# Performance work log

Measured on AMD Instinct MI355X. Metric: run time of the kernel, lower is better.

## Reference

```python
import jax, jax.numpy as jnp
import numpy as np

N_NODES = 20000
NEG_SLOPE = 0.2  # PyG GATConv default leaky_relu slope


def segment_softmax(e, dst, num_segments):
    # e: [E, H] edge logits, softmax over edges sharing the same dst node
    m = jax.ops.segment_max(e, dst, num_segments=num_segments)
    ex = jnp.exp(e - m[dst])
    s = jax.ops.segment_sum(ex, dst, num_segments=num_segments)
    return ex / (s[dst] + 1e-16)


def gat_conv(x, src, dst, W, att_src, att_dst, bias, concat):
    # PyG GATConv (add_self_loops handled by caller). W: [Fin, H*C], att_*: [H, C]
    N = x.shape[0]
    H, C = att_src.shape
    h = (x @ W).reshape(N, H, C)
    a_src = jnp.einsum('nhc,hc->nh', h, att_src)  # [N, H]
    a_dst = jnp.einsum('nhc,hc->nh', h, att_dst)
    e = jax.nn.leaky_relu(a_src[src] + a_dst[dst], NEG_SLOPE)  # [E, H]
    alpha = segment_softmax(e, dst, N)
    msg = alpha[:, :, None] * h[src]  # [E, H, C]
    out = jax.ops.segment_sum(msg, dst, num_segments=N)  # [N, H, C]
    out = out.reshape(N, H * C) if concat else out.mean(axis=1)
    return out + bias


def add_self_loops(edge_index, num_nodes):
    loops = jnp.arange(num_nodes, dtype=edge_index.dtype)
    src = jnp.concatenate([edge_index[0], loops])
    dst = jnp.concatenate([edge_index[1], loops])
    return src, dst


def setup_inputs() -> dict:
    key = jax.random.key(0)
    ks = jax.random.split(key, 24)
    Fin, Hd, Hh, C2, Md = 1280, 256, 4, 128, 1024

    def w(k, shape, fan_in):
        return (jax.random.normal(k, shape, jnp.float32) * (1.0 / np.sqrt(fan_in))).astype(jnp.float32)

    return {
        'x': jax.random.normal(ks[0], (N_NODES, Fin), jnp.float32),
        'edge_index': jax.random.randint(ks[1], (2, 200000), 0, N_NODES, jnp.int32),
        'mutation_idx': 12345,
        'mutation_site_diff': jax.random.normal(ks[2], (1, Md), jnp.float32),
        # mutation_diff_processor: 1024 -> 128 -> 128
        'W_mut1': w(ks[3], (Md, 128), Md), 'b_mut1': jnp.zeros((128,), jnp.float32),
        'W_mut2': w(ks[4], (128, 128), 128), 'b_mut2': jnp.zeros((128,), jnp.float32),
        # GATConv1: Fin -> 256, 4 heads, concat
        'gat1_W': w(ks[5], (Fin, Hh * Hd), Fin),
        'gat1_as': w(ks[6], (Hh, Hd), Hd), 'gat1_ad': w(ks[7], (Hh, Hd), Hd),
        'gat1_b': jnp.zeros((Hh * Hd,), jnp.float32),
        # GATConv2: 1024 -> 128, 1 head
        'gat2_W': w(ks[8], (Hh * Hd, C2), Hh * Hd),
        'gat2_as': w(ks[9], (1, C2), C2), 'gat2_ad': w(ks[10], (1, C2), C2),
        'gat2_b': jnp.zeros((C2,), jnp.float32),
        # binding_predictor: 256 -> 128 -> 32 -> 1
        'W_p1': w(ks[11], (C2 + 128, 128), C2 + 128), 'b_p1': jnp.zeros((128,), jnp.float32),
        'W_p2': w(ks[12], (128, 32), 128), 'b_p2': jnp.zeros((32,), jnp.float32),
        'W_p3': w(ks[13], (32, 1), 32), 'b_p3': jnp.zeros((1,), jnp.float32),
    }


def reference(x, edge_index, mutation_idx, mutation_site_diff,
              W_mut1, b_mut1, W_mut2, b_mut2,
              gat1_W, gat1_as, gat1_ad, gat1_b,
              gat2_W, gat2_as, gat2_ad, gat2_b,
              W_p1, b_p1, W_p2, b_p2, W_p3, b_p3):
    src, dst = add_self_loops(edge_index, x.shape[0])
    # mutation diff MLP (dropout = identity at eval)
    pmd = jax.nn.relu(mutation_site_diff @ W_mut1 + b_mut1) @ W_mut2 + b_mut2
    h = jax.nn.relu(gat_conv(x, src, dst, gat1_W, gat1_as, gat1_ad, gat1_b, concat=True))
    h = jax.nn.relu(gat_conv(h, src, dst, gat2_W, gat2_as, gat2_ad, gat2_b, concat=False))
    feat = h[mutation_idx:mutation_idx + 1]  # [1, 128]
    z = jnp.concatenate([feat, pmd], axis=-1)
    z = jax.nn.relu(z @ W_p1 + b_p1)
    z = jax.nn.relu(z @ W_p2 + b_p2)
    return z @ W_p3 + b_p3
```

## Files before the change

### kernel.cpp

```cpp
#include <hip/hip_runtime.h>
#include <hip/hip_bf16.h>

#define NNODES 20000
#define NE_RAW 200000
#define NE_TOT 220000
#define MAX1   128
#define MAXE1  4096
#define MAXE2  256
#define FIN    1280
#define FH     1024
#define NHEAD  4
#define C2     128
#define CAPE   512
#define KCK    64
#define NKC    20
#define INIT_B 79
#define A_B    160
#define PMD_B  4
#define D_B    160

__device__ __forceinline__ float lrelu(float x){ return x >= 0.f ? x : 0.2f * x; }

__global__ __launch_bounds__(256) void k_init_a(
    const float* __restrict__ W1, const float* __restrict__ as1,
    const float* __restrict__ ad1,
    const float* __restrict__ msd, const float* __restrict__ Wm1,
    const float* __restrict__ bm1,
    int* cnt, int* slot1, float* __restrict__ w_att, float* __restrict__ r1){
  int t = threadIdx.x, b = blockIdx.x;
  if (b < INIT_B){
    int i = b * 256 + t;
    if (i < NNODES) slot1[i] = -1;
    if (i < 8) cnt[i] = 0;
    return;
  }
  if (b >= INIT_B + A_B){
    __shared__ float red[256];
    int pb  = b - INIT_B - A_B;
    int col = pb * 32 + (t & 31);
    int sl  = t >> 5;
    float s = 0.f;
    for (int k = sl * 128; k < sl * 128 + 128; ++k)
      s += msd[k] * Wm1[k * C2 + col];
    red[t] = s;
    __syncthreads();
    if (t < 32){
      float v = 0.f;
      #pragma unroll
      for (int q = 0; q < 8; ++q) v += red[q * 32 + t];
      v += bm1[col];
      r1[col] = v > 0.f ? v : 0.f;
    }
    return;
  }
  __shared__ float red[4][8];
  int kbase = (b - INIT_B) * 8;
  int w = t >> 6, lane = t & 63;
  float av0 = as1[t], av1 = as1[t + 256], av2 = as1[t + 512], av3 = as1[t + 768];
  float dv0 = ad1[t], dv1 = ad1[t + 256], dv2 = ad1[t + 512], dv3 = ad1[t + 768];
  for (int rr = 0; rr < 8; ++rr){
    int k = kbase + rr;
    const float* Wr = W1 + (long)k * FH;
    float w0 = Wr[t], w1 = Wr[t + 256], w2 = Wr[t + 512], w3 = Wr[t + 768];
    float v[8] = { w0*av0, w1*av1, w2*av2, w3*av3, w0*dv0, w1*dv1, w2*dv2, w3*dv3 };
    #pragma unroll
    for (int q = 0; q < 8; ++q){
      float s = v[q];
      #pragma unroll
      for (int o = 32; o; o >>= 1) s += __shfl_xor(s, o, 64);
      if (lane == 0) red[w][q] = s;
      __syncthreads();
      if (t == 0) w_att[k * 8 + q] = red[0][q] + red[1][q] + red[2][q] + red[3][q];
      __syncthreads();
    }
  }
}

__global__ void k_scan1(const int* __restrict__ ei, const int* __restrict__ mip,
                        int* cnt, int* slot1, int* S1, int* E2){
  int e0 = (blockIdx.x * 256 + threadIdx.x) * 4;
  if (e0 >= NE_TOT) return;
  int mi = mip[0];
  int s[4], d[4], n = 0;
  if (e0 + 3 < NE_RAW){
    int4 s4 = *(const int4*)(ei + e0);
    int4 d4 = *(const int4*)(ei + NE_RAW + e0);
    s[0]=s4.x; s[1]=s4.y; s[2]=s4.z; s[3]=s4.w;
    d[0]=d4.x; d[1]=d4.y; d[2]=d4.z; d[3]=d4.w;
    n = 4;
  } else {
    for (int q = 0; q < 4; ++q){
      int e = e0 + q;
      if (e >= NE_TOT) break;
      if (e < NE_RAW){ s[n] = ei[e]; d[n] = ei[NE_RAW + e]; }
      else { s[n] = e - NE_RAW; d[n] = s[n]; }
      ++n;
    }
  }
  for (int q = 0; q < n; ++q){
    if (d[q] != mi) continue;
    int p = atomicAdd(&cnt[3], 1);
    if (p < MAXE2) E2[p] = s[q];
    if (atomicCAS(&slot1[s[q]], -1, -9) == -1){
      int idx = atomicAdd(&cnt[0], 1);
      if (idx < MAX1){ S1[idx] = s[q]; slot1[s[q]] = idx; }
    }
  }
}

__global__ void k_scan2(const int* __restrict__ ei, int* cnt,
                        const int* __restrict__ slot1, int* E1s, int* E1d){
  int e0 = (blockIdx.x * 256 + threadIdx.x) * 4;
  if (e0 >= NE_TOT) return;
  int s[4], d[4], n = 0;
  if (e0 + 3 < NE_RAW){
    int4 s4 = *(const int4*)(ei + e0);
    int4 d4 = *(const int4*)(ei + NE_RAW + e0);
    s[0]=s4.x; s[1]=s4.y; s[2]=s4.z; s[3]=s4.w;
    d[0]=d4.x; d[1]=d4.y; d[2]=d4.z; d[3]=d4.w;
    n = 4;
  } else {
    for (int q = 0; q < 4; ++q){
      int e = e0 + q;
      if (e >= NE_TOT) break;
      if (e < NE_RAW){ s[n] = ei[e]; d[n] = ei[NE_RAW + e]; }
      else { s[n] = e - NE_RAW; d[n] = s[n]; }
      ++n;
    }
  }
  for (int q = 0; q < n; ++q){
    if (slot1[d[q]] < 0) continue;
    int p = atomicAdd(&cnt[2], 1);
    if (p < MAXE1){ E1s[p] = s[q]; E1d[p] = d[q]; }
  }
}

__global__ __launch_bounds__(256) void k_bc(
    const float* __restrict__ x, const float* __restrict__ w_att,
    const int* __restrict__ cnt, const int* __restrict__ S1,
    const int* __restrict__ E1s, const int* __restrict__ E1d,
    float* __restrict__ X1){
  __shared__ int   lsrc[CAPE];
  __shared__ float ev[NHEAD][CAPE];
  __shared__ float adml[NHEAD];
  __shared__ float redl[4][4];
  __shared__ int   scnt;
  int t = threadIdx.x, w = t >> 6, lane = t & 63;
  int n1  = cnt[0]; if (n1  > MAX1)  n1  = MAX1;
  int nE1 = cnt[2]; if (nE1 > MAXE1) nE1 = MAXE1;
  for (int j = blockIdx.x; j < n1; j += gridDim.x){
    int s = S1[j];
    __syncthreads();
    if (t == 0) scnt = 0;
    __syncthreads();
    for (int e = t; e < nE1; e += 256){
      if (E1d[e] == s){
        int q = atomicAdd(&scnt, 1);
        if (q < CAPE) lsrc[q] = E1s[e];
      }
    }
    __syncthreads();
    int ce = scnt; if (ce > CAPE) ce = CAPE;
    {
      const float* xs = x + (long)s * FIN;
      float a0=0.f, a1=0.f, a2=0.f, a3=0.f;
      #pragma unroll
      for (int i = 0; i < 5; ++i){
        int k = t + 256 * i;
        float xv = xs[k];
        float4 wd = *(const float4*)(w_att + k * 8 + 4);
        a0 += xv * wd.x; a1 += xv * wd.y; a2 += xv * wd.z; a3 += xv * wd.w;
      }
      float v[4] = { a0, a1, a2, a3 };
      #pragma unroll
      for (int q = 0; q < 4; ++q){
        float sv = v[q];
        #pragma unroll
        for (int o = 32; o; o >>= 1) sv += __shfl_xor(sv, o, 64);
        if (lane == 0) redl[w][q] = sv;
      }
      __syncthreads();
      if (t < 4) adml[t] = redl[0][t] + redl[1][t] + redl[2][t] + redl[3][t];
      __syncthreads();
    }
    for (int e = w; e < ce; e += 4){
      const float* xe = x + (long)lsrc[e] * FIN;
      float b0=0.f, b1v=0.f, b2v=0.f, b3v=0.f;
      #pragma unroll 4
      for (int i = 0; i < 20; ++i){
        int k = lane + 64 * i;
        float xv = xe[k];
        float4 ws = *(const float4*)(w_att + k * 8);
        b0 += xv * ws.x; b1v += xv * ws.y; b2v += xv * ws.z; b3v += xv * ws.w;
      }
      #pragma unroll
      for (int o = 32; o; o >>= 1){
        b0  += __shfl_xor(b0, o, 64);  b1v += __shfl_xor(b1v, o, 64);
        b2v += __shfl_xor(b2v, o, 64); b3v += __shfl_xor(b3v, o, 64);
      }
      if (lane == 0){ ev[0][e]=b0; ev[1][e]=b1v; ev[2][e]=b2v; ev[3][e]=b3v; }
    }
    __syncthreads();
    {
      float ad = adml[w];
      float m = -3.4e38f;
      for (int e = lane; e < ce; e += 64){
        float v = lrelu(ev[w][e] + ad);
        ev[w][e] = v;
        m = fmaxf(m, v);
      }
      #pragma unroll
      for (int o = 32; o; o >>= 1) m = fmaxf(m, __shfl_xor(m, o, 64));
      float ssum = 0.f;
      for (int e = lane; e < ce; e += 64){
        float a2 = expf(ev[w][e] - m);
        ev[w][e] = a2;
        ssum += a2;
      }
      #pragma unroll
      for (int o = 32; o; o >>= 1) ssum += __shfl_xor(ssum, o, 64);
      float inv = 1.f / (ssum + 1e-16f);
      for (int e = lane; e < ce; e += 64) ev[w][e] *= inv;
    }
    __syncthreads();
    {
      float acc[20];
      #pragma unroll
      for (int i = 0; i < 20; ++i) acc[i] = 0.f;
      for (int e = 0; e < ce; ++e){
        float al = ev[w][e];
        const float* xe = x + (long)lsrc[e] * FIN;
        #pragma unroll
        for (int i = 0; i < 20; ++i) acc[i] += al * xe[lane + 64 * i];
      }
      float* X1p = X1 + ((long)j * NHEAD + w) * FIN;
      #pragma unroll
      for (int i = 0; i < 20; ++i) X1p[lane + 64 * i] = acc[i];
    }
    __syncthreads();
  }
}

__global__ __launch_bounds__(256) void k_d(
    const float* __restrict__ X1, const float* __restrict__ W1,
    const int* __restrict__ cnt, float* __restrict__ hpart){
  __shared__ float Wl[KCK][128];
  __shared__ float Xl[KCK][16];
  int t = threadIdx.x, bid = blockIdx.x;
  int ct = bid & 7, kc = bid >> 3;
  int head = ct >> 1;
  int k0 = kc * KCK, c0 = ct * 128;
  int n1 = cnt[0]; if (n1 > MAX1) n1 = MAX1;
  for (int idx = t; idx < 2048; idx += 256){
    int r = idx >> 5, c4 = idx & 31;
    *(float4*)&Wl[r][c4 * 4] = *(const float4*)(W1 + (long)(k0 + r) * FH + c0 + c4 * 4);
  }
  int nRG = (n1 + 15) >> 4;
  int cth = t & 31, rth = t >> 5;
  for (int rg = 0; rg < nRG; ++rg){
    int r0 = rg * 16;
    __syncthreads();
    {
      int r = t & 15, kq = t >> 4;
      float4 v = make_float4(0.f, 0.f, 0.f, 0.f);
      if (r0 + r < n1)
        v = *(const float4*)(X1 + ((long)(r0 + r) * NHEAD + head) * FIN + k0 + kq * 4);
      Xl[kq * 4 + 0][r] = v.x;
      Xl[kq * 4 + 1][r] = v.y;
      Xl[kq * 4 + 2][r] = v.z;
      Xl[kq * 4 + 3][r] = v.w;
    }
    __syncthreads();
    float4 A0 = make_float4(0.f,0.f,0.f,0.f), A1 = A0;
    #pragma unroll 4
    for (int k = 0; k < KCK; ++k){
      float4 wv = *(const float4*)&Wl[k][cth * 4];
      float x0 = Xl[k][rth * 2], x1 = Xl[k][rth * 2 + 1];
      A0.x += x0 * wv.x; A0.y += x0 * wv.y; A0.z += x0 * wv.z; A0.w += x0 * wv.w;
      A1.x += x1 * wv.x; A1.y += x1 * wv.y; A1.z += x1 * wv.z; A1.w += x1 * wv.w;
    }
    int rb = r0 + rth * 2;
    float* dp = hpart + ((long)kc * MAX1 + rb) * FH + c0 + cth * 4;
    if (rb < n1)     *(float4*)(dp)      = A0;
    if (rb + 1 < n1) *(float4*)(dp + FH) = A1;
  }
}

__global__ __launch_bounds__(1024) void k_e(
    const float* __restrict__ hpart, const float* __restrict__ b1,
    const float* __restrict__ W2, const int* __restrict__ cnt,
    float* __restrict__ gb){
  __shared__ float h1row[FH];
  __shared__ float part[8][C2];
  int t = threadIdx.x;
  int n1 = cnt[0]; if (n1 > MAX1) n1 = MAX1;
  for (int j = blockIdx.x; j < n1; j += gridDim.x){
    __syncthreads();
    if (t < 256){
      float4 s = make_float4(0.f, 0.f, 0.f, 0.f);
      #pragma unroll
      for (int kc = 0; kc < NKC; ++kc){
        float4 v = *(const float4*)(hpart + ((long)kc * MAX1 + j) * FH + 4 * t);
        s.x += v.x; s.y += v.y; s.z += v.z; s.w += v.w;
      }
      float4 bv = *(const float4*)(b1 + 4 * t);
      s.x += bv.x; s.y += bv.y; s.z += bv.z; s.w += bv.w;
      s.x = s.x > 0.f ? s.x : 0.f;
      s.y = s.y > 0.f ? s.y : 0.f;
      s.z = s.z > 0.f ? s.z : 0.f;
      s.w = s.w > 0.f ? s.w : 0.f;
      *(float4*)(h1row + 4 * t) = s;
    }
    __syncthreads();
    {
      int col = t & 127, sl = t >> 7;
      const float* Wp = W2 + (long)(sl * 128) * C2 + col;
      const float* hp = h1row + sl * 128;
      float g = 0.f;
      #pragma unroll 16
      for (int k = 0; k < 128; ++k) g += hp[k] * Wp[(long)k * C2];
      part[sl][col] = g;
    }
    __syncthreads();
    if (t < C2){
      float s8 = 0.f;
      #pragma unroll
      for (int q = 0; q < 8; ++q) s8 += part[q][t];
      gb[j * C2 + t] = s8;
    }
  }
}

__global__ __launch_bounds__(512) void k_final(
    const int* __restrict__ mip, const int* __restrict__ cnt,
    const int* __restrict__ slot1, const int* __restrict__ E2,
    const float* __restrict__ gb,
    const float* __restrict__ as2, const float* __restrict__ ad2,
    const float* __restrict__ b2,
    const float* __restrict__ r1,
    const float* __restrict__ Wm2, const float* __restrict__ bm2,
    const float* __restrict__ Wp1, const float* __restrict__ bp1,
    const float* __restrict__ Wp2, const float* __restrict__ bp2,
    const float* __restrict__ Wp3, const float* __restrict__ bp3,
    float* __restrict__ out){
  __shared__ float al[MAXE2];
  __shared__ int   jl[MAXE2];
  __shared__ float feat[C2], r2s[C2], z1s[C2], z2s[32];
  __shared__ float p4[4][C2];
  __shared__ float p16[16][32];
  int t = threadIdx.x;
  int mi  = mip[0];
  int jmi = slot1[mi];
  int ne2 = cnt[3]; if (ne2 > MAXE2) ne2 = MAXE2;
  for (int k = t; k < ne2; k += 512) jl[k] = slot1[E2[k]];
  __syncthreads();
  int w = t >> 6, lane = t & 63;
  {
    int c = lane * 2;
    float v = gb[jmi * C2 + c] * ad2[c] + gb[jmi * C2 + c + 1] * ad2[c + 1];
    #pragma unroll
    for (int o = 32; o; o >>= 1) v += __shfl_xor(v, o, 64);
    float adv = v;
    for (int k = w; k < ne2; k += 8){
      int jj = jl[k];
      float u = gb[jj * C2 + c] * as2[c] + gb[jj * C2 + c + 1] * as2[c + 1];
      #pragma unroll
      for (int o = 32; o; o >>= 1) u += __shfl_xor(u, o, 64);
      if (lane == 0) al[k] = lrelu(u + adv);
    }
  }
  __syncthreads();
  if (t < 64){
    float m = -3.4e38f;
    for (int k = t; k < ne2; k += 64) m = fmaxf(m, al[k]);
    #pragma unroll
    for (int o = 32; o; o >>= 1) m = fmaxf(m, __shfl_xor(m, o, 64));
    float s = 0.f;
    for (int k = t; k < ne2; k += 64){
      float a2 = expf(al[k] - m);
      al[k] = a2;
      s += a2;
    }
    #pragma unroll
    for (int o = 32; o; o >>= 1) s += __shfl_xor(s, o, 64);
    float inv = 1.f / (s + 1e-16f);
    for (int k = t; k < ne2; k += 64) al[k] *= inv;
  }
  __syncthreads();
  int col = t & 127, sub = t >> 7;
  {
    float pr = 0.f;
    #pragma unroll 8
    for (int k = sub * 32; k < sub * 32 + 32; ++k) pr += r1[k] * Wm2[k * C2 + col];
    p4[sub][col] = pr;
    if (t < C2){
      float acc = 0.f;
      for (int k = 0; k < ne2; ++k) acc += al[k] * gb[jl[k] * C2 + t];
      float v = acc + b2[t];
      feat[t] = v > 0.f ? v : 0.f;
    }
  }
  __syncthreads();
  if (t < C2) r2s[t] = p4[0][t] + p4[1][t] + p4[2][t] + p4[3][t] + bm2[t];
  __syncthreads();
  {
    float acc = 0.f;
    #pragma unroll 8
    for (int k = sub * 64; k < sub * 64 + 64; ++k){
      float zv = (k < C2) ? feat[k] : r2s[k - C2];
      acc += zv * Wp1[k * C2 + col];
    }
    p4[sub][col] = acc;
  }
  __syncthreads();
  if (t < C2){
    float v = p4[0][t] + p4[1][t] + p4[2][t] + p4[3][t] + bp1[t];
    z1s[t] = v > 0.f ? v : 0.f;
  }
  __syncthreads();
  {
    int c2 = t & 31, sl = t >> 5;
    float acc = 0.f;
    #pragma unroll
    for (int k = sl * 8; k < sl * 8 + 8; ++k) acc += z1s[k] * Wp2[k * 32 + c2];
    p16[sl][c2] = acc;
  }
  __syncthreads();
  if (t < 32){
    float s = 0.f;
    #pragma unroll
    for (int q = 0; q < 16; ++q) s += p16[q][t];
    float v = s + bp2[t];
    z2s[t] = v > 0.f ? v : 0.f;
  }
  __syncthreads();
  if (t == 0){
    float acc = 0.f;
    for (int k = 0; k < 32; ++k) acc += z2s[k] * Wp3[k];
    out[0] = acc + bp3[0];
  }
}

extern "C" void kernel_launch(void* const* d_in, const int* in_sizes, int n_in,
                              void* d_out, int out_size, void* d_ws, size_t ws_size,
                              hipStream_t stream){
  const float* x   = (const float*)d_in[0];
  const int*   ei  = (const int*)d_in[1];
  const int*   mip = (const int*)d_in[2];
  const float* msd = (const float*)d_in[3];
  const float* Wm1 = (const float*)d_in[4];
  const float* bm1 = (const float*)d_in[5];
  const float* Wm2 = (const float*)d_in[6];
  const float* bm2 = (const float*)d_in[7];
  const float* W1  = (const float*)d_in[8];
  const float* as1 = (const float*)d_in[9];
  const float* ad1 = (const float*)d_in[10];
  const float* b1  = (const float*)d_in[11];
  const float* W2  = (const float*)d_in[12];
  const float* as2 = (const float*)d_in[13];
  const float* ad2 = (const float*)d_in[14];
  const float* b2  = (const float*)d_in[15];
  const float* Wp1 = (const float*)d_in[16];
  const float* bp1 = (const float*)d_in[17];
  const float* Wp2 = (const float*)d_in[18];
  const float* bp2 = (const float*)d_in[19];
  const float* Wp3 = (const float*)d_in[20];
  const float* bp3 = (const float*)d_in[21];
  float* out = (float*)d_out;

  char* q = (char*)d_ws;
  auto alloc = [&](size_t bytes) -> void* {
    void* r = (void*)q;
    q += (bytes + 255) & ~(size_t)255;
    return r;
  };
  int* cnt   = (int*)alloc(8 * 4);
  int* slot1 = (int*)alloc(NNODES * 4);
  int* S1    = (int*)alloc(MAX1 * 4);
  int* E1s   = (int*)alloc(MAXE1 * 4);
  int* E1d   = (int*)alloc(MAXE1 * 4);
  int* E2    = (int*)alloc(MAXE2 * 4);
  float* w_att = (float*)alloc((size_t)FIN * 8 * 4);
  float* X1    = (float*)alloc((size_t)MAX1 * NHEAD * FIN * 4);
  float* hpart = (float*)alloc((size_t)NKC * MAX1 * FH * 4);
  float* gb    = (float*)alloc(MAX1 * C2 * 4);
  float* r1    = (float*)alloc(C2 * 4);

  k_init_a<<<INIT_B + A_B + PMD_B, 256, 0, stream>>>(W1, as1, ad1, msd, Wm1, bm1,
                                                     cnt, slot1, w_att, r1);
  k_scan1<<<(NE_TOT + 1023) / 1024, 256, 0, stream>>>(ei, mip, cnt, slot1, S1, E2);
  k_scan2<<<(NE_TOT + 1023) / 1024, 256, 0, stream>>>(ei, cnt, slot1, E1s, E1d);
  k_bc   <<<32, 256, 0, stream>>>(x, w_att, cnt, S1, E1s, E1d, X1);
  k_d    <<<D_B, 256, 0, stream>>>(X1, W1, cnt, hpart);
  k_e    <<<16, 1024, 0, stream>>>(hpart, b1, W2, cnt, gb);
  k_final<<<1, 512, 0, stream>>>(mip, cnt, slot1, E2, gb, as2, ad2, b2, r1,
                                 Wm2, bm2, Wp1, bp1, Wp2, bp2, Wp3, bp3, out);
}
```

Baseline: 68.97 us.

## Replace global scan kernels with per-block E2 buckets and in-kernel neighbor rescans

Merges the init, scan1 and scan2 kernels into a single pre kernel. That kernel writes per-block buckets of in-edges to the mutation node. Each later kernel rebuilds the deduplicated S1 list serially in one thread, and k_bc rescans the whole edge list per S1 node instead of using a prebuilt E1 list. The split-K partial buffer is replaced by atomicAdd into a zeroed h1, removing the reduction loop in k_e. This cuts launches and the global atomics and slot table. In exchange it adds redundant full edge scans in k_bc, fewer k_bc blocks, serial dedup work in every kernel, and nondeterministic float atomics.

```diff
diff --git a/kernel.cpp b/kernel.cpp
--- a/kernel.cpp
+++ b/kernel.cpp
@@ -3,9 +3,7 @@
 
 #define NNODES 20000
 #define NE_RAW 200000
-#define NE_TOT 220000
 #define MAX1   128
-#define MAXE1  4096
 #define MAXE2  256
 #define FIN    1280
 #define FH     1024
@@ -14,29 +12,107 @@
 #define CAPE   512
 #define KCK    64
 #define NKC    20
-#define INIT_B 79
-#define A_B    160
-#define PMD_B  4
+#define E2CAP  32
+#define NSCAN  196
+#define NREG   (NSCAN + 1)
+#define B_WATT 40
+#define B_PMD  4
+#define B_HZ   16
+#define PRE_B  (B_WATT + NSCAN + B_PMD + B_HZ)
 #define D_B    160
 
 __device__ __forceinline__ float lrelu(float x){ return x >= 0.f ? x : 0.2f * x; }
 
-__global__ __launch_bounds__(256) void k_init_a(
+__device__ int derive_S1(const int* __restrict__ E2cnt, const int* __restrict__ E2raw,
+                         int* S1l){
+  int n1 = 0;
+  for (int b = 0; b < NREG; ++b){
+    int c = E2cnt[b];
+    if (c < 0) c = 0; if (c > E2CAP) c = E2CAP;
+    for (int s = 0; s < c; ++s){
+      int v = E2raw[b * E2CAP + s];
+      bool found = false;
+      for (int k = 0; k < n1; ++k) if (S1l[k] == v){ found = true; break; }
+      if (!found && n1 < MAX1) S1l[n1++] = v;
+    }
+  }
+  return n1;
+}
+
+__global__ __launch_bounds__(256) void k_pre(
+    const int* __restrict__ ei, const int* __restrict__ mip,
     const float* __restrict__ W1, const float* __restrict__ as1,
     const float* __restrict__ ad1,
     const float* __restrict__ msd, const float* __restrict__ Wm1,
     const float* __restrict__ bm1,
-    int* cnt, int* slot1, float* __restrict__ w_att, float* __restrict__ r1){
-  int t = threadIdx.x, b = blockIdx.x;
-  if (b < INIT_B){
-    int i = b * 256 + t;
-    if (i < NNODES) slot1[i] = -1;
-    if (i < 8) cnt[i] = 0;
+    int* __restrict__ E2cnt, int* __restrict__ E2raw,
+    float* __restrict__ w_att, float* __restrict__ r1,
+    float4* __restrict__ h1z){
+  int b = blockIdx.x, t = threadIdx.x;
+  if (b < B_WATT){
+    int w = t >> 6, lane = t & 63;
+    float av[16], dv[16];
+    #pragma unroll
+    for (int i = 0; i < 16; ++i){ av[i] = as1[lane + 64 * i]; dv[i] = ad1[lane + 64 * i]; }
+    int kbase = (b * 4 + w) * 8;
+    for (int rr = 0; rr < 8; ++rr){
+      int k = kbase + rr;
+      const float* Wr = W1 + (long)k * FH;
+      float wv[16];
+      #pragma unroll
+      for (int i = 0; i < 16; ++i) wv[i] = Wr[lane + 64 * i];
+      float s[8];
+      #pragma unroll
+      for (int h = 0; h < 4; ++h){
+        float sa = 0.f, sd = 0.f;
+        #pragma unroll
+        for (int i = 4 * h; i < 4 * h + 4; ++i){ sa += wv[i] * av[i]; sd += wv[i] * dv[i]; }
+        s[h] = sa; s[4 + h] = sd;
+      }
+      #pragma unroll
+      for (int q = 0; q < 8; ++q){
+        float v = s[q];
+        #pragma unroll
+        for (int o = 32; o; o >>= 1) v += __shfl_xor(v, o, 64);
+        if (lane == 0) w_att[(long)k * 8 + q] = v;
+      }
+    }
     return;
   }
-  if (b >= INIT_B + A_B){
+  if (b < B_WATT + NSCAN){
+    __shared__ int lcnt;
+    __shared__ int lbuf[E2CAP];
+    int sb = b - B_WATT;
+    if (t == 0) lcnt = 0;
+    __syncthreads();
+    int mi = mip[0];
+    int e0 = sb * 1024 + t * 4;
+    if (e0 < NE_RAW){
+      int4 s4 = *(const int4*)(ei + e0);
+      int4 d4 = *(const int4*)(ei + NE_RAW + e0);
+      int ss[4] = { s4.x, s4.y, s4.z, s4.w };
+      int dd[4] = { d4.x, d4.y, d4.z, d4.w };
+      #pragma unroll
+      for (int q = 0; q < 4; ++q){
+        if (dd[q] == mi){
+          int p = atomicAdd(&lcnt, 1);
+          if (p < E2CAP) lbuf[p] = ss[q];
+        }
+      }
+    }
+    __syncthreads();
+    int c = lcnt; if (c > E2CAP) c = E2CAP;
+    if (t == 0) E2cnt[sb] = c;
+    if (t < c) E2raw[sb * E2CAP + t] = lbuf[t];
+    return;
+  }
+  if (b < B_WATT + NSCAN + B_PMD){
     __shared__ float red[256];
-    int pb  = b - INIT_B - A_B;
+    int pb  = b - B_WATT - NSCAN;
+    if (pb == 0 && t == 0){
+      E2cnt[NSCAN] = 1;
+      E2raw[NSCAN * E2CAP] = mip[0];
+    }
     int col = pb * 32 + (t & 31);
     int sl  = t >> 5;
     float s = 0.f;
@@ -53,111 +129,52 @@
     }
     return;
   }
-  __shared__ float red[4][8];
-  int kbase = (b - INIT_B) * 8;
-  int w = t >> 6, lane = t & 63;
-  float av0 = as1[t], av1 = as1[t + 256], av2 = as1[t + 512], av3 = as1[t + 768];
-  float dv0 = ad1[t], dv1 = ad1[t + 256], dv2 = ad1[t + 512], dv3 = ad1[t + 768];
-  for (int rr = 0; rr < 8; ++rr){
-    int k = kbase + rr;
-    const float* Wr = W1 + (long)k * FH;
-    float w0 = Wr[t], w1 = Wr[t + 256], w2 = Wr[t + 512], w3 = Wr[t + 768];
-    float v[8] = { w0*av0, w1*av1, w2*av2, w3*av3, w0*dv0, w1*dv1, w2*dv2, w3*dv3 };
-    #pragma unroll
-    for (int q = 0; q < 8; ++q){
-      float s = v[q];
-      #pragma unroll
-      for (int o = 32; o; o >>= 1) s += __shfl_xor(s, o, 64);
-      if (lane == 0) red[w][q] = s;
-      __syncthreads();
-      if (t == 0) w_att[k * 8 + q] = red[0][q] + red[1][q] + red[2][q] + red[3][q];
-      __syncthreads();
-    }
-  }
-}
-
-__global__ void k_scan1(const int* __restrict__ ei, const int* __restrict__ mip,
-                        int* cnt, int* slot1, int* S1, int* E2){
-  int e0 = (blockIdx.x * 256 + threadIdx.x) * 4;
-  if (e0 >= NE_TOT) return;
-  int mi = mip[0];
-  int s[4], d[4], n = 0;
-  if (e0 + 3 < NE_RAW){
-    int4 s4 = *(const int4*)(ei + e0);
-    int4 d4 = *(const int4*)(ei + NE_RAW + e0);
-    s[0]=s4.x; s[1]=s4.y; s[2]=s4.z; s[3]=s4.w;
-    d[0]=d4.x; d[1]=d4.y; d[2]=d4.z; d[3]=d4.w;
-    n = 4;
-  } else {
-    for (int q = 0; q < 4; ++q){
-      int e = e0 + q;
-      if (e >= NE_TOT) break;
-      if (e < NE_RAW){ s[n] = ei[e]; d[n] = ei[NE_RAW + e]; }
-      else { s[n] = e - NE_RAW; d[n] = s[n]; }
-      ++n;
-    }
-  }
-  for (int q = 0; q < n; ++q){
-    if (d[q] != mi) continue;
-    int p = atomicAdd(&cnt[3], 1);
-    if (p < MAXE2) E2[p] = s[q];
-    if (atomicCAS(&slot1[s[q]], -1, -9) == -1){
-      int idx = atomicAdd(&cnt[0], 1);
-      if (idx < MAX1){ S1[idx] = s[q]; slot1[s[q]] = idx; }
-    }
-  }
-}
-
-__global__ void k_scan2(const int* __restrict__ ei, int* cnt,
-                        const int* __restrict__ slot1, int* E1s, int* E1d){
-  int e0 = (blockIdx.x * 256 + threadIdx.x) * 4;
-  if (e0 >= NE_TOT) return;
-  int s[4], d[4], n = 0;
-  if (e0 + 3 < NE_RAW){
-    int4 s4 = *(const int4*)(ei + e0);
-    int4 d4 = *(const int4*)(ei + NE_RAW + e0);
-    s[0]=s4.x; s[1]=s4.y; s[2]=s4.z; s[3]=s4.w;
-    d[0]=d4.x; d[1]=d4.y; d[2]=d4.z; d[3]=d4.w;
-    n = 4;
-  } else {
-    for (int q = 0; q < 4; ++q){
-      int e = e0 + q;
-      if (e >= NE_TOT) break;
-      if (e < NE_RAW){ s[n] = ei[e]; d[n] = ei[NE_RAW + e]; }
-      else { s[n] = e - NE_RAW; d[n] = s[n]; }
-      ++n;
-    }
-  }
-  for (int q = 0; q < n; ++q){
-    if (slot1[d[q]] < 0) continue;
-    int p = atomicAdd(&cnt[2], 1);
-    if (p < MAXE1){ E1s[p] = s[q]; E1d[p] = d[q]; }
+  {
+    int zb = b - B_WATT - NSCAN - B_PMD;
+    float4 z = make_float4(0.f, 0.f, 0.f, 0.f);
+    int base = zb * 2048 + t;
+    #pragma unroll
+    for (int i = 0; i < 8; ++i) h1z[base + 256 * i] = z;
   }
 }
 
 __global__ __launch_bounds__(256) void k_bc(
-    const float* __restrict__ x, const float* __restrict__ w_att,
-    const int* __restrict__ cnt, const int* __restrict__ S1,
-    const int* __restrict__ E1s, const int* __restrict__ E1d,
+    const float* __restrict__ x, const int* __restrict__ ei,
+    const float* __restrict__ w_att,
+    const int* __restrict__ E2cnt, const int* __restrict__ E2raw,
     float* __restrict__ X1){
+  __shared__ int   S1l[MAX1];
+  __shared__ int   n1s;
   __shared__ int   lsrc[CAPE];
   __shared__ float ev[NHEAD][CAPE];
   __shared__ float adml[NHEAD];
   __shared__ float redl[4][4];
   __shared__ int   scnt;
   int t = threadIdx.x, w = t >> 6, lane = t & 63;
-  int n1  = cnt[0]; if (n1  > MAX1)  n1  = MAX1;
-  int nE1 = cnt[2]; if (nE1 > MAXE1) nE1 = MAXE1;
+  if (t == 0) n1s = derive_S1(E2cnt, E2raw, S1l);
+  __syncthreads();
+  int n1 = n1s;
   for (int j = blockIdx.x; j < n1; j += gridDim.x){
-    int s = S1[j];
+    int s = S1l[j];
     __syncthreads();
     if (t == 0) scnt = 0;
     __syncthreads();
-    for (int e = t; e < nE1; e += 256){
-      if (E1d[e] == s){
-        int q = atomicAdd(&scnt, 1);
-        if (q < CAPE) lsrc[q] = E1s[e];
-      }
+    for (int base = t * 4; base < NE_RAW; base += 1024){
+      int4 s4 = *(const int4*)(ei + base);
+      int4 d4 = *(const int4*)(ei + NE_RAW + base);
+      int ss[4] = { s4.x, s4.y, s4.z, s4.w };
+      int dd[4] = { d4.x, d4.y, d4.z, d4.w };
+      #pragma unroll
+      for (int q = 0; q < 4; ++q){
+        if (dd[q] == s){
+          int p = atomicAdd(&scnt, 1);
+          if (p < CAPE) lsrc[p] = ss[q];
+        }
+      }
+    }
+    if (t == 0){
+      int p = atomicAdd(&scnt, 1);
+      if (p < CAPE) lsrc[p] = s;
     }
     __syncthreads();
     int ce = scnt; if (ce > CAPE) ce = CAPE;
@@ -243,18 +260,23 @@
 
 __global__ __launch_bounds__(256) void k_d(
     const float* __restrict__ X1, const float* __restrict__ W1,
-    const int* __restrict__ cnt, float* __restrict__ hpart){
+    const int* __restrict__ E2cnt, const int* __restrict__ E2raw,
+    float* __restrict__ h1){
   __shared__ float Wl[KCK][128];
   __shared__ float Xl[KCK][16];
+  __shared__ int   S1l[MAX1];
+  __shared__ int   n1s;
   int t = threadIdx.x, bid = blockIdx.x;
+  if (t == 0) n1s = derive_S1(E2cnt, E2raw, S1l);
   int ct = bid & 7, kc = bid >> 3;
   int head = ct >> 1;
   int k0 = kc * KCK, c0 = ct * 128;
-  int n1 = cnt[0]; if (n1 > MAX1) n1 = MAX1;
   for (int idx = t; idx < 2048; idx += 256){
     int r = idx >> 5, c4 = idx & 31;
     *(float4*)&Wl[r][c4 * 4] = *(const float4*)(W1 + (long)(k0 + r) * FH + c0 + c4 * 4);
   }
+  __syncthreads();
+  int n1 = n1s;
   int nRG = (n1 + 15) >> 4;
   int cth = t & 31, rth = t >> 5;
   for (int rg = 0; rg < nRG; ++rg){
@@ -280,29 +302,36 @@
       A1.x += x1 * wv.x; A1.y += x1 * wv.y; A1.z += x1 * wv.z; A1.w += x1 * wv.w;
     }
     int rb = r0 + rth * 2;
-    float* dp = hpart + ((long)kc * MAX1 + rb) * FH + c0 + cth * 4;
-    if (rb < n1)     *(float4*)(dp)      = A0;
-    if (rb + 1 < n1) *(float4*)(dp + FH) = A1;
+    float* dp = h1 + (long)rb * FH + c0 + cth * 4;
+    if (rb < n1){
+      atomicAdd(dp + 0, A0.x); atomicAdd(dp + 1, A0.y);
+      atomicAdd(dp + 2, A0.z); atomicAdd(dp + 3, A0.w);
+    }
+    if (rb + 1 < n1){
+      float* d1 = dp + FH;
+      atomicAdd(d1 + 0, A1.x); atomicAdd(d1 + 1, A1.y);
+      atomicAdd(d1 + 2, A1.z); atomicAdd(d1 + 3, A1.w);
+    }
   }
 }
 
 __global__ __launch_bounds__(1024) void k_e(
-    const float* __restrict__ hpart, const float* __restrict__ b1,
-    const float* __restrict__ W2, const int* __restrict__ cnt,
+    const float* __restrict__ h1, const float* __restrict__ b1,
+    const float* __restrict__ W2,
+    const int* __restrict__ E2cnt, const int* __restrict__ E2raw,
     float* __restrict__ gb){
   __shared__ float h1row[FH];
   __shared__ float part[8][C2];
+  __shared__ int   S1l[MAX1];
+  __shared__ int   n1s;
   int t = threadIdx.x;
-  int n1 = cnt[0]; if (n1 > MAX1) n1 = MAX1;
+  if (t == 0) n1s = derive_S1(E2cnt, E2raw, S1l);
+  __syncthreads();
+  int n1 = n1s;
   for (int j = blockIdx.x; j < n1; j += gridDim.x){
     __syncthreads();
     if (t < 256){
-      float4 s = make_float4(0.f, 0.f, 0.f, 0.f);
-      #pragma unroll
-      for (int kc = 0; kc < NKC; ++kc){
-        float4 v = *(const float4*)(hpart + ((long)kc * MAX1 + j) * FH + 4 * t);
-        s.x += v.x; s.y += v.y; s.z += v.z; s.w += v.w;
-      }
+      float4 s = *(const float4*)(h1 + (long)j * FH + 4 * t);
       float4 bv = *(const float4*)(b1 + 4 * t);
       s.x += bv.x; s.y += bv.y; s.z += bv.z; s.w += bv.w;
       s.x = s.x > 0.f ? s.x : 0.f;
@@ -332,8 +361,8 @@
 }
 
 __global__ __launch_bounds__(512) void k_final(
-    const int* __restrict__ mip, const int* __restrict__ cnt,
-    const int* __restrict__ slot1, const int* __restrict__ E2,
+    const int* __restrict__ mip,
+    const int* __restrict__ E2cnt, const int* __restrict__ E2raw,
     const float* __restrict__ gb,
     const float* __restrict__ as2, const float* __restrict__ ad2,
     const float* __restrict__ b2,
@@ -345,15 +374,33 @@
     float* __restrict__ out){
   __shared__ float al[MAXE2];
   __shared__ int   jl[MAXE2];
+  __shared__ int   S1l[MAX1];
+  __shared__ int   meta[2];
   __shared__ float feat[C2], r2s[C2], z1s[C2], z2s[32];
   __shared__ float p4[4][C2];
   __shared__ float p16[16][32];
   int t = threadIdx.x;
-  int mi  = mip[0];
-  int jmi = slot1[mi];
-  int ne2 = cnt[3]; if (ne2 > MAXE2) ne2 = MAXE2;
-  for (int k = t; k < ne2; k += 512) jl[k] = slot1[E2[k]];
-  __syncthreads();
+  if (t == 0){
+    int n1 = derive_S1(E2cnt, E2raw, S1l);
+    int ne2 = 0;
+    for (int b = 0; b < NREG; ++b){
+      int c = E2cnt[b];
+      if (c < 0) c = 0; if (c > E2CAP) c = E2CAP;
+      for (int s = 0; s < c; ++s){
+        int v = E2raw[b * E2CAP + s];
+        if (ne2 < MAXE2){
+          int idx = 0;
+          for (int k = 0; k < n1; ++k) if (S1l[k] == v){ idx = k; break; }
+          jl[ne2++] = idx;
+        }
+      }
+    }
+    int mi = mip[0], jmi = 0;
+    for (int k = 0; k < n1; ++k) if (S1l[k] == mi){ jmi = k; break; }
+    meta[0] = ne2; meta[1] = jmi;
+  }
+  __syncthreads();
+  int ne2 = meta[0], jmi = meta[1];
   int w = t >> 6, lane = t & 63;
   {
     int c = lane * 2;
@@ -474,25 +521,19 @@
     q += (bytes + 255) & ~(size_t)255;
     return r;
   };
-  int* cnt   = (int*)alloc(8 * 4);
-  int* slot1 = (int*)alloc(NNODES * 4);
-  int* S1    = (int*)alloc(MAX1 * 4);
-  int* E1s   = (int*)alloc(MAXE1 * 4);
-  int* E1d   = (int*)alloc(MAXE1 * 4);
-  int* E2    = (int*)alloc(MAXE2 * 4);
+  int*   E2cnt = (int*)alloc(NREG * 4);
+  int*   E2raw = (int*)alloc((size_t)NREG * E2CAP * 4);
   float* w_att = (float*)alloc((size_t)FIN * 8 * 4);
   float* X1    = (float*)alloc((size_t)MAX1 * NHEAD * FIN * 4);
-  float* hpart = (float*)alloc((size_t)NKC * MAX1 * FH * 4);
+  float* h1    = (float*)alloc((size_t)MAX1 * FH * 4);
   float* gb    = (float*)alloc(MAX1 * C2 * 4);
   float* r1    = (float*)alloc(C2 * 4);
 
-  k_init_a<<<INIT_B + A_B + PMD_B, 256, 0, stream>>>(W1, as1, ad1, msd, Wm1, bm1,
-                                                     cnt, slot1, w_att, r1);
-  k_scan1<<<(NE_TOT + 1023) / 1024, 256, 0, stream>>>(ei, mip, cnt, slot1, S1, E2);
-  k_scan2<<<(NE_TOT + 1023) / 1024, 256, 0, stream>>>(ei, cnt, slot1, E1s, E1d);
-  k_bc   <<<32, 256, 0, stream>>>(x, w_att, cnt, S1, E1s, E1d, X1);
-  k_d    <<<D_B, 256, 0, stream>>>(X1, W1, cnt, hpart);
-  k_e    <<<16, 1024, 0, stream>>>(hpart, b1, W2, cnt, gb);
-  k_final<<<1, 512, 0, stream>>>(mip, cnt, slot1, E2, gb, as2, ad2, b2, r1,
+  k_pre  <<<PRE_B, 256, 0, stream>>>(ei, mip, W1, as1, ad1, msd, Wm1, bm1,
+                                     E2cnt, E2raw, w_att, r1, (float4*)h1);
+  k_bc   <<<16, 256, 0, stream>>>(x, ei, w_att, E2cnt, E2raw, X1);
+  k_d    <<<D_B, 256, 0, stream>>>(X1, W1, E2cnt, E2raw, h1);
+  k_e    <<<16, 1024, 0, stream>>>(h1, b1, W2, E2cnt, E2raw, gb);
+  k_final<<<1, 512, 0, stream>>>(mip, E2cnt, E2raw, gb, as2, ad2, b2, r1,
                                  Wm2, bm2, Wp1, bp1, Wp2, bp2, Wp3, bp3, out);
 }
```

After: 199.9 us. 2.9x slower.
